# Kernel optimization log

Hardware: AMD Instinct MI355X
Metric: run time of the kernel (lower is better)

Reference implementation:

```python
import jax, jax.numpy as jnp
import numpy as np

B, H, W, DIM = 1, 256, 256, 192
HEADS = 6
K, DIL = 7, 2            # NAttention kernel / dilation
WS, DF = 8, 2            # stripe window size, anchor down factor
AWS = WS // DF           # anchor window size (4)
N1, N2 = WS * WS, AWS * AWS
L = H * W
CPB_HID = 512


def _nbr(size, k, d):
    # 1D neighborhood-attention neighbor indices with dilation (edge-clamped)
    i = np.arange(size); g = i % d; p = i // d
    gsize = size // d  # d divides size
    start = np.clip(p - k // 2, 0, gsize - k)
    nbr_p = start[:, None] + np.arange(k)[None, :]
    nbr = g[:, None] + d * nbr_p                    # absolute key index
    rb = nbr_p - p[:, None] + (k - 1)               # rpb index in [0, 2k-2]
    return nbr.astype(np.int32), rb.astype(np.int32)

NBR_H, RB_H = _nbr(H, K, DIL)
NBR_W, RB_W = _nbr(W, K, DIL)


def _na_attention(q, k, v, rpb):
    # q,k,v: (B, heads, H, W, hd); rpb: (heads, 2K-1, 2K-1)
    bias = rpb[:, RB_H, :]                          # (heads,H,K,2K-1)
    bias = jnp.take(bias, RB_W, axis=3)             # (heads,H,K,W,K)
    bias = jnp.transpose(bias, (0, 1, 3, 2, 4))     # (heads,H,W,K,K)
    logits = []
    for ki in range(K):
        kh = jnp.take(k, NBR_H[:, ki], axis=2)
        for kj in range(K):
            khw = jnp.take(kh, NBR_W[:, kj], axis=3)
            logits.append(jnp.einsum('bnhwc,bnhwc->bnhw', q, khw))
    a = jnp.stack(logits, axis=-1).reshape(*q.shape[:4], K, K) + bias[None]
    a = jax.nn.softmax(a.reshape(*q.shape[:4], K * K), axis=-1).reshape(*q.shape[:4], K, K)
    out = jnp.zeros_like(q)
    for ki in range(K):
        vh = jnp.take(v, NBR_H[:, ki], axis=2)
        for kj in range(K):
            vhw = jnp.take(vh, NBR_W[:, kj], axis=3)
            out = out + a[..., ki, kj, None] * vhw
    return out

na_attention = jax.checkpoint(_na_attention)


def window_partition(x, ws):
    b, h, w, c = x.shape
    x = x.reshape(b, h // ws, ws, w // ws, ws, c)
    return jnp.transpose(x, (0, 1, 3, 2, 4, 5)).reshape(-1, ws * ws, c)


def window_reverse(x, ws, h, w):
    c = x.shape[-1]
    b = x.shape[0] // ((h // ws) * (w // ws))
    x = x.reshape(b, h // ws, w // ws, ws, ws, c)
    return jnp.transpose(x, (0, 1, 3, 2, 4, 5)).reshape(b, h, w, c)


def _l2n(x):
    n = jnp.linalg.norm(x, axis=-1, keepdims=True)
    return x / jnp.maximum(n, 1e-12)


def _affine(attn, table, index, ls, w1, b1, w2):
    # attn: (Bw, heads, Na, Nb)
    attn = attn * jnp.exp(jnp.minimum(ls, float(np.log(100.0))))[None]
    bt = jax.nn.relu(table.reshape(-1, 2) @ w1 + b1) @ w2           # (T, heads)
    bias = bt[index.reshape(-1)].reshape(index.shape[0], index.shape[1], HEADS)
    bias = 16.0 * jax.nn.sigmoid(jnp.transpose(bias, (2, 0, 1)))    # (heads,Na,Nb)
    return attn + bias[None]


def _cos_attn(q, k, v, table, index, ls, w1, b1, w2):
    attn = jnp.einsum('bhnc,bhmc->bhnm', _l2n(q), _l2n(k))
    attn = jax.nn.softmax(_affine(attn, table, index, ls, w1, b1, w2), axis=-1)
    return attn @ v


def _forward(x, h_size, w_size, table, index_a2w, index_w2a, qkv_w, qkv_b,
             anchor_dw_w, anchor_dw_b, anchor_pw_w, anchor_pw_b,
             na_qkv_w, na_qkv_b, na_after_w, na_after_b, na_rpb,
             ls1, cpb1_w1, cpb1_b1, cpb1_w2, ls2, cpb2_w1, cpb2_b1, cpb2_w2,
             proj_w, proj_b):
    Bx, Lx, C = x.shape
    Hs, Ws_ = int(h_size), int(w_size)
    qkv = x @ qkv_w + qkv_b                     # (B,L,3C)
    half = C * 3 // 2
    qkv_window, qkv_stripe = qkv[..., :half], qkv[..., half:]
    # anchor projection: depthwise conv (k=DF+1, stride=DF) + pointwise
    xi = x.reshape(Bx, Hs, Ws_, C)
    a = jax.lax.conv_general_dilated(
        xi, anchor_dw_w, (DF, DF), ((1, 1), (1, 1)),
        dimension_numbers=('NHWC', 'HWIO', 'NHWC'), feature_group_count=C) + anchor_dw_b
    a = a @ anchor_pw_w + anchor_pw_b           # (B, H/DF, W/DF, C//2)
    # ---- neighborhood attention branch ----
    hd = C // HEADS
    xw = qkv_window.reshape(Bx, Hs, Ws_, half)
    q2 = (xw @ na_qkv_w + na_qkv_b).reshape(Bx, Hs, Ws_, 3, HEADS, hd)
    q2 = jnp.transpose(q2, (3, 0, 4, 1, 2, 5))  # (3,B,heads,H,W,hd)
    qn, kn, vn = q2[0] * hd ** -0.5, q2[1], q2[2]
    xna = na_attention(qn, kn, vn, na_rpb)
    xna = jnp.transpose(xna, (0, 2, 3, 1, 4)).reshape(Bx, Hs, Ws_, C)
    xna = (xna @ na_after_w + na_after_b).reshape(Bx, Lx, C // 2)
    # ---- anchor stripe attention branch ----
    qs = window_partition(qkv_stripe.reshape(Bx, Hs, Ws_, half), WS)  # (Bw,N1,1.5C)
    an = window_partition(a, AWS)                                     # (Bw,N2,C//2)
    Bw = qs.shape[0]
    hs = C // 2 // HEADS
    q3 = jnp.transpose(qs.reshape(Bw, N1, 3, HEADS, hs), (2, 0, 3, 1, 4))
    q_s, k_s, v_s = q3[0], q3[1], q3[2]
    an = jnp.transpose(an.reshape(Bw, N2, HEADS, hs), (0, 2, 1, 3))
    x1 = _cos_attn(an, k_s, v_s, table, index_a2w, ls1, cpb1_w1, cpb1_b1, cpb1_w2)
    x2 = _cos_attn(q_s, an, x1, table, index_w2a, ls2, cpb2_w1, cpb2_b1, cpb2_w2)
    x2 = jnp.transpose(x2, (0, 2, 1, 3)).reshape(Bw, N1, C // 2)
    xs = window_reverse(x2, WS, Hs, Ws_).reshape(Bx, Lx, C // 2)
    return jnp.concatenate([xna, xs], axis=-1) @ proj_w + proj_b


def setup_inputs() -> dict:
    key = jax.random.key(0)
    ks = jax.random.split(key, 16)
    f = lambda i, shp, s=0.02: jax.random.normal(ks[i], shp, dtype=jnp.float32) * s
    x = jax.random.normal(ks[0], (B, L, DIM), dtype=jnp.float32)
    # swin-v2 style normalized log-spaced relative coords table
    rc = np.arange(-(WS - 1), WS, dtype=np.float32) / (WS - 1)
    t = np.stack(np.meshgrid(rc, rc, indexing='ij'), axis=-1)[None]
    table = jnp.asarray(np.sign(t) * np.log2(1 + np.abs(t) * 8) / 3.0, dtype=jnp.float32)
    wc = np.arange(WS); ac = np.arange(AWS) * DF
    cw = np.stack(np.meshgrid(wc, wc, indexing='ij'), -1).reshape(-1, 2)
    ca = np.stack(np.meshgrid(ac, ac, indexing='ij'), -1).reshape(-1, 2)
    def _idx(c1, c2):
        d = c1[:, None, :] - c2[None, :, :]
        return jnp.asarray((d[..., 0] + WS - 1) * (2 * WS - 1) + (d[..., 1] + WS - 1), dtype=jnp.int32)
    return {
        'x': x, 'h_size': H, 'w_size': W, 'table': table,
        'index_a2w': _idx(ca, cw), 'index_w2a': _idx(cw, ca),
        'qkv_w': f(1, (DIM, 3 * DIM)), 'qkv_b': jnp.zeros((3 * DIM,), jnp.float32),
        'anchor_dw_w': f(2, (DF + 1, DF + 1, 1, DIM), 0.1),
        'anchor_dw_b': jnp.zeros((DIM,), jnp.float32),
        'anchor_pw_w': f(3, (DIM, DIM // 2)), 'anchor_pw_b': jnp.zeros((DIM // 2,), jnp.float32),
        'na_qkv_w': f(4, (3 * DIM // 2, 3 * DIM)), 'na_qkv_b': jnp.zeros((3 * DIM,), jnp.float32),
        'na_after_w': f(5, (DIM, DIM // 2)), 'na_after_b': jnp.zeros((DIM // 2,), jnp.float32),
        'na_rpb': f(6, (HEADS, 2 * K - 1, 2 * K - 1)),
        'ls1': jnp.log(10.0) * jnp.ones((HEADS, 1, 1), jnp.float32),
        'cpb1_w1': f(7, (2, CPB_HID), 0.1), 'cpb1_b1': jnp.zeros((CPB_HID,), jnp.float32),
        'cpb1_w2': f(8, (CPB_HID, HEADS), 0.1),
        'ls2': jnp.log(10.0) * jnp.ones((HEADS, 1, 1), jnp.float32),
        'cpb2_w1': f(9, (2, CPB_HID), 0.1), 'cpb2_b1': jnp.zeros((CPB_HID,), jnp.float32),
        'cpb2_w2': f(10, (CPB_HID, HEADS), 0.1),
        'proj_w': f(11, (DIM, DIM)), 'proj_b': jnp.zeros((DIM,), jnp.float32),
    }


def reference(x, h_size, w_size, table, index_a2w, index_w2a, qkv_w, qkv_b,
              anchor_dw_w, anchor_dw_b, anchor_pw_w, anchor_pw_b,
              na_qkv_w, na_qkv_b, na_after_w, na_after_b, na_rpb,
              ls1, cpb1_w1, cpb1_b1, cpb1_w2, ls2, cpb2_w1, cpb2_b1, cpb2_w2,
              proj_w, proj_b):
    return _forward(x, h_size, w_size, table, index_a2w, index_w2a, qkv_w, qkv_b,
                    anchor_dw_w, anchor_dw_b, anchor_pw_w, anchor_pw_b,
                    na_qkv_w, na_qkv_b, na_after_w, na_after_b, na_rpb,
                    ls1, cpb1_w1, cpb1_b1, cpb1_w2, ls2, cpb2_w1, cpb2_b1, cpb2_w2,
                    proj_w, proj_b)
```

## Files before the change

kernel.cpp:

```cpp
#include <hip/hip_runtime.h>
#include <math.h>


typedef unsigned short bf16_t;
typedef __attribute__((ext_vector_type(8))) short short8;
typedef __attribute__((ext_vector_type(4))) float f32x4;

__device__ inline float bf2f(bf16_t v) { return __uint_as_float((unsigned)v << 16); }
__device__ inline bf16_t f2bf(float f) {
    unsigned u = __float_as_uint(f);
    unsigned r = (u + 0x7fffu + ((u >> 16) & 1u)) >> 16;
    return (bf16_t)r;
}
__device__ inline float cvt(float v) { return v; }
__device__ inline float cvt(bf16_t v) { return bf2f(v); }
__device__ inline void sto(float* p, float v) { *p = v; }
__device__ inline void sto(bf16_t* p, float v) { *p = f2bf(v); }

__device__ inline void ld_bf8(const bf16_t* p, float* d) {
    uint4 r = *(const uint4*)p;
    d[0] = __uint_as_float(r.x << 16); d[1] = __uint_as_float(r.x & 0xffff0000u);
    d[2] = __uint_as_float(r.y << 16); d[3] = __uint_as_float(r.y & 0xffff0000u);
    d[4] = __uint_as_float(r.z << 16); d[5] = __uint_as_float(r.z & 0xffff0000u);
    d[6] = __uint_as_float(r.w << 16); d[7] = __uint_as_float(r.w & 0xffff0000u);
}
__device__ inline unsigned pk2(float a, float b) {
    return (unsigned)f2bf(a) | ((unsigned)f2bf(b) << 16);
}

template <int KD, int NA, typename TO>
__global__ __launch_bounds__(256) void mfma_gemm_k(
    const bf16_t* __restrict__ A, const bf16_t* __restrict__ Bt,
    const float* __restrict__ bias, TO* __restrict__ C,
    int lda, int ldb, int ldc)
{
    const int t = threadIdx.x;
    const int lane = t & 63, wave = t >> 6;
    const int wr = wave >> 1, wc = wave & 1;
    const int m0 = blockIdx.y * 128 + wr * 64;
    const int n0 = blockIdx.x * 96 + wc * 48;
    const int lm = lane & 15;
    const int q  = lane >> 4;

    f32x4 acc[4][3] = {};
    const bf16_t* ap = A + (size_t)(m0 + lm) * lda + q * 8;
    const bf16_t* bp = Bt + (size_t)(n0 + lm) * ldb + q * 8;

#pragma unroll
    for (int k0 = 0; k0 < KD; k0 += 32) {
        short8 af[4], bf[3];
#pragma unroll
        for (int mi = 0; mi < 4; mi++)
            af[mi] = *(const short8*)(ap + (size_t)(mi * 16) * lda + k0);
#pragma unroll
        for (int ni = 0; ni < 3; ni++)
            bf[ni] = *(const short8*)(bp + (size_t)(ni * 16) * ldb + k0);
#pragma unroll
        for (int mi = 0; mi < 4; mi++)
#pragma unroll
            for (int ni = 0; ni < 3; ni++)
                acc[mi][ni] = __builtin_amdgcn_mfma_f32_16x16x32_bf16(
                    af[mi], bf[ni], acc[mi][ni], 0, 0, 0);
    }

#pragma unroll
    for (int mi = 0; mi < 4; mi++) {
#pragma unroll
        for (int ni = 0; ni < 3; ni++) {
            int col = n0 + ni * 16 + lm;
            float bv = bias[col];
            if (NA) {
                int which = col / 192;
                int hh = (col % 192) / 32;
                int d  = col % 32;
                size_t pbase = ((size_t)which * 6 + hh) * ((size_t)65536 * 32) + d;
#pragma unroll
                for (int r = 0; r < 4; r++) {
                    int row = m0 + mi * 16 + q * 4 + r;
                    int ii = row >> 8, jj = row & 255;
                    int par = ((ii & 1) << 1) | (jj & 1);
                    int pix = par * 16384 + (ii >> 1) * 128 + (jj >> 1);
                    sto(&C[pbase + (size_t)pix * 32], acc[mi][ni][r] + bv);
                }
            } else {
#pragma unroll
                for (int r = 0; r < 4; r++) {
                    int row = m0 + mi * 16 + q * 4 + r;
                    sto(&C[(size_t)row * ldc + col], acc[mi][ni][r] + bv);
                }
            }
        }
    }
}

__global__ __launch_bounds__(256) void cvt_bf16_k(
    const float* __restrict__ src, bf16_t* __restrict__ dst, int n8)
{
    int tid = blockIdx.x * 256 + threadIdx.x;
    if (tid >= n8) return;
    float4 a = ((const float4*)src)[tid * 2];
    float4 b = ((const float4*)src)[tid * 2 + 1];
    uint4 o;
    o.x = pk2(a.x, a.y); o.y = pk2(a.z, a.w);
    o.z = pk2(b.x, b.y); o.w = pk2(b.z, b.w);
    ((uint4*)dst)[tid] = o;
}

__global__ __launch_bounds__(256) void tcvt_k(
    const float* __restrict__ W, bf16_t* __restrict__ Wt,
    int Kd, int N, int ld, int coloff)
{
    int tid = blockIdx.x * 256 + threadIdx.x;
    if (tid >= Kd * N) return;
    int k = tid % Kd, n = tid / Kd;
    Wt[tid] = f2bf(W[(size_t)k * ld + coloff + n]);
}

__global__ __launch_bounds__(256) void tpose_qkvw_k(
    const float* __restrict__ W, float* __restrict__ WT)
{
    int tid = blockIdx.x * 256 + threadIdx.x;
    if (tid >= 288 * 192) return;
    int k = tid % 192, j = tid / 192;
    WT[tid] = W[(size_t)k * 576 + j];
}

__global__ __launch_bounds__(256) void fold_wna_t_k(
    const float* __restrict__ qkv_wT, const float* __restrict__ na_qkv_w,
    bf16_t* __restrict__ Wna_t)
{
    int tid = blockIdx.x * 256 + threadIdx.x;
    if (tid >= 576 * 192) return;
    int k = tid % 192, n = tid / 192;
    float acc = 0.f;
    for (int j = 0; j < 288; j++)
        acc += qkv_wT[j * 192 + k] * na_qkv_w[j * 576 + n];
    Wna_t[tid] = f2bf(acc);
}

__global__ __launch_bounds__(256) void fold_bna_k(
    const float* __restrict__ qkv_b, const float* __restrict__ na_qkv_w,
    const float* __restrict__ na_qkv_b, float* __restrict__ bna)
{
    int j = blockIdx.x * 256 + threadIdx.x;
    if (j >= 576) return;
    float acc = na_qkv_b[j];
    for (int k = 0; k < 288; k++)
        acc += qkv_b[k] * na_qkv_w[k * 576 + j];
    bna[j] = acc;
}

__global__ __launch_bounds__(256) void cpb_k(
    const float* __restrict__ table, const float* __restrict__ w1,
    const float* __restrict__ b1, const float* __restrict__ w2,
    float* __restrict__ bt)
{
    int tid = blockIdx.x * 256 + threadIdx.x;
    if (tid >= 225 * 6) return;
    int h = tid % 6, t = tid / 6;
    float t0 = table[t * 2], t1 = table[t * 2 + 1];
    float acc = 0.f;
    for (int m = 0; m < 512; m++) {
        float hv = t0 * w1[m] + t1 * w1[512 + m] + b1[m];
        hv = fmaxf(hv, 0.f);
        acc += hv * w2[m * 6 + h];
    }
    bt[tid] = acc;
}

__global__ __launch_bounds__(256) void sigb_k(
    const float* __restrict__ bt, const int* __restrict__ idx,
    float* __restrict__ bp)
{
    int tid = blockIdx.x * 256 + threadIdx.x;
    if (tid >= 6144) return;
    int h = tid >> 10, p = tid & 1023;
    bp[tid] = 16.0f / (1.0f + __expf(-bt[idx[p] * 6 + h]));
}

__global__ __launch_bounds__(256) void sigb1T_k(
    const float* __restrict__ bt, const int* __restrict__ idx,
    float* __restrict__ bp)
{
    int tid = blockIdx.x * 256 + threadIdx.x;
    if (tid >= 6144) return;
    int h = tid >> 10, p = tid & 1023;
    int m = p >> 4, n2 = p & 15;
    bp[tid] = 16.0f / (1.0f + __expf(-bt[idx[n2 * 64 + m] * 6 + h]));
}

#define BM 64
#define BN 64
#define BKK 16
template <typename TA, typename TO>
__global__ __launch_bounds__(256) void gemm_k(
    const TA* __restrict__ A, const float* __restrict__ B,
    const float* __restrict__ bias, TO* __restrict__ C,
    int M, int N, int Kd, int lda, int ldb, int ldc)
{
    __shared__ float As[BKK][BM + 1];
    __shared__ float Bs[BKK][BN + 1];
    const int t  = threadIdx.x;
    const int tx = t & 15, ty = t >> 4;
    const int m0 = blockIdx.y * BM, n0 = blockIdx.x * BN;
    float acc[4][4] = {};

    for (int k0 = 0; k0 < Kd; k0 += BKK) {
#pragma unroll
        for (int i = 0; i < 4; i++) {
            int m = (t >> 4) + i * 16;
            int k = t & 15;
            int gm = m0 + m, gk = k0 + k;
            As[k][m] = (gm < M && gk < Kd) ? cvt(A[(size_t)gm * lda + gk]) : 0.f;
        }
#pragma unroll
        for (int i = 0; i < 4; i++) {
            int k = (t >> 6) + i * 4;
            int n = t & 63;
            int gk = k0 + k, gn = n0 + n;
            Bs[k][n] = (gk < Kd && gn < N) ? B[(size_t)gk * ldb + gn] : 0.f;
        }
        __syncthreads();
#pragma unroll
        for (int k = 0; k < BKK; k++) {
            float a[4], b[4];
#pragma unroll
            for (int i = 0; i < 4; i++) a[i] = As[k][ty * 4 + i];
#pragma unroll
            for (int j = 0; j < 4; j++) b[j] = Bs[k][tx * 4 + j];
#pragma unroll
            for (int i = 0; i < 4; i++)
#pragma unroll
                for (int j = 0; j < 4; j++) acc[i][j] += a[i] * b[j];
        }
        __syncthreads();
    }
#pragma unroll
    for (int i = 0; i < 4; i++) {
        int gm = m0 + ty * 4 + i;
        if (gm >= M) continue;
#pragma unroll
        for (int j = 0; j < 4; j++) {
            int gn = n0 + tx * 4 + j;
            if (gn >= N) continue;
            sto(&C[(size_t)gm * ldc + gn], acc[i][j] + bias[gn]);
        }
    }
}

__global__ __launch_bounds__(256) void dwconv_k(
    const float* __restrict__ x, const float* __restrict__ w,
    const float* __restrict__ b, float* __restrict__ adw)
{
    int tid = blockIdx.x * 256 + threadIdx.x;
    if (tid >= 16384 * 48) return;
    int c4 = tid % 48;
    int p = tid / 48;
    int ow = p & 127, oh = p >> 7;
    int c = c4 * 4;
    float4 s = *(const float4*)(b + c);
#pragma unroll
    for (int kh = 0; kh < 3; kh++) {
        int ih = oh * 2 - 1 + kh;
        if (ih < 0 || ih >= 256) continue;
#pragma unroll
        for (int kw = 0; kw < 3; kw++) {
            int iw = ow * 2 - 1 + kw;
            if (iw < 0 || iw >= 256) continue;
            float4 xv = *(const float4*)(x + (size_t)(ih * 256 + iw) * 192 + c);
            float4 wv = *(const float4*)(w + (kh * 3 + kw) * 192 + c);
            s.x += xv.x * wv.x; s.y += xv.y * wv.y;
            s.z += xv.z * wv.z; s.w += xv.w * wv.w;
        }
    }
    *(float4*)(adw + (size_t)p * 192 + c) = s;
}

__global__ __launch_bounds__(256) void na_attn_k(
    const bf16_t* __restrict__ nap, const float* __restrict__ rpb,
    bf16_t* __restrict__ outp)
{
    __shared__ float rpb_s[176];
    __shared__ __align__(16) unsigned P_s[4][16][20];

    const int t = threadIdx.x;
    const int wv = t >> 6, lane = t & 63;
    const int lm = lane & 15, lq = lane >> 4;
    const int z = blockIdx.z;
    const int h = z >> 2, par = z & 3;

    if (t < 169) rpb_s[t] = rpb[h * 169 + t];
    __syncthreads();

    const int pi  = blockIdx.y;
    const int pj0 = blockIdx.x * 64 + wv * 16;
    const int si  = min(max(pi - 3, 0), 121);
    const int rbh0 = si - pi + 6;
    const int c0  = min(max(pj0 - 3, 0), 121) & ~7;

    const size_t plane = (size_t)65536 * 32;
    const size_t poff  = (size_t)(par * 16384) * 32;
    const bf16_t* qpl = nap + (size_t)h * plane + poff;
    const bf16_t* kpl = nap + (size_t)(6 + h) * plane + poff;
    const bf16_t* vpl = nap + (size_t)(12 + h) * plane + poff;

    const short8 qf = *(const short8*)(qpl + ((size_t)(pi * 128 + pj0 + lm)) * 32 + lq * 8);

    int offc[4][2]; bool vm[4][2];
#pragma unroll
    for (int r = 0; r < 4; r++) {
        int q = lq * 4 + r, pj = pj0 + q;
        int sj = min(max(pj - 3, 0), 121);
#pragma unroll
        for (int t2 = 0; t2 < 2; t2++) {
            int c = c0 + 2 * lm + t2;
            vm[r][t2] = (c >= sj) && (c <= sj + 6);
            offc[r][t2] = min(max(c - pj + 6, 0), 12);
        }
    }
    const int kc0 = min(c0 + 2 * lm,     127) * 64;
    const int kc1 = min(c0 + 2 * lm + 1, 127) * 64;
    int vcoff[8];
#pragma unroll
    for (int i = 0; i < 8; i++) vcoff[i] = min(c0 + lq * 8 + i, 127) * 64;

    const float scale = 0.17677669529663687f;
    f32x4 o0 = {}, o1 = {};
    float sums[4] = {0.f, 0.f, 0.f, 0.f};
    const f32x4 zz = {};

#pragma unroll 2
    for (int rr = 0; rr < 7; rr++) {
        const size_t rb2 = (size_t)((si + rr) * 128) * 64;
        const char* krow = (const char*)kpl + rb2;
        const char* vrow = (const char*)vpl + rb2;

        short8 kf0 = *(const short8*)(krow + kc0 + lq * 16);
        short8 kf1 = *(const short8*)(krow + kc1 + lq * 16);
        f32x4 s0 = __builtin_amdgcn_mfma_f32_16x16x32_bf16(qf, kf0, zz, 0, 0, 0);
        f32x4 s1 = __builtin_amdgcn_mfma_f32_16x16x32_bf16(qf, kf1, zz, 0, 0, 0);

        const float* br = rpb_s + (rbh0 + rr) * 13;
        float e0[4], e1[4];
#pragma unroll
        for (int r = 0; r < 4; r++) {
            float a0 = __expf(fmaf(s0[r], scale, br[offc[r][0]]));
            float a1 = __expf(fmaf(s1[r], scale, br[offc[r][1]]));
            a0 = vm[r][0] ? a0 : 0.f;
            a1 = vm[r][1] ? a1 : 0.f;
            e0[r] = a0; e1[r] = a1;
            sums[r] += a0 + a1;
        }
#pragma unroll
        for (int r = 0; r < 4; r++) {
            unsigned pr;
            asm("v_cvt_pk_bf16_f32 %0, %1, %2" : "=v"(pr) : "v"(e0[r]), "v"(e1[r]));
            P_s[wv][lq * 4 + r][lm] = pr;
        }
        const short8 pf = *(const short8*)((const bf16_t*)P_s[wv][lm] + lq * 8);

        short8 vf0, vf1;
        const char* v0b = vrow + lm * 2;
        const char* v1b = vrow + 32 + lm * 2;
#pragma unroll
        for (int i = 0; i < 8; i++) {
            ((bf16_t*)&vf0)[i] = *(const bf16_t*)(v0b + vcoff[i]);
            ((bf16_t*)&vf1)[i] = *(const bf16_t*)(v1b + vcoff[i]);
        }
        o0 = __builtin_amdgcn_mfma_f32_16x16x32_bf16(pf, vf0, o0, 0, 0, 0);
        o1 = __builtin_amdgcn_mfma_f32_16x16x32_bf16(pf, vf1, o1, 0, 0, 0);
    }

#pragma unroll
    for (int r = 0; r < 4; r++) {
        float s = sums[r];
        s += __shfl_xor(s, 1, 64);
        s += __shfl_xor(s, 2, 64);
        s += __shfl_xor(s, 4, 64);
        s += __shfl_xor(s, 8, 64);
        sums[r] = 1.0f / s;
    }

    const int gi = par >> 1, gj = par & 1;
    const int i0 = pi * 2 + gi;
    bf16_t* ob = outp + ((size_t)i0 * 256 + gj) * 192 + h * 32 + lm;
#pragma unroll
    for (int r = 0; r < 4; r++) {
        int q = lq * 4 + r;
        size_t px = (size_t)(pj0 + q) * 2 * 192;
        ob[px]      = f2bf(o0[r] * sums[r]);
        ob[px + 16] = f2bf(o1[r] * sums[r]);
    }
}

__global__ __launch_bounds__(256) void attn1_k(
    const float* __restrict__ apw,
    const bf16_t* __restrict__ qkvs,
    const float* __restrict__ b1pT,
    const float* __restrict__ ls1,
    float* __restrict__ x1)
{
    __shared__ float bT_s[1024];
    __shared__ __align__(16) unsigned P_s[4][16][36];

    const int t = threadIdx.x;
    const int wv = t >> 6, lane = t & 63;
    const int lm = lane & 15, lq = lane >> 4;
    const int h = blockIdx.y;
    const int w = blockIdx.x * 4 + wv;
    const int wi = w >> 5, wj = w & 31;

#pragma unroll
    for (int i = 0; i < 4; i++) bT_s[i * 256 + t] = b1pT[h * 1024 + i * 256 + t];
    __syncthreads();

    const float scale = __expf(fminf(ls1[h], 4.605170185988091f));

    short8 af = {};
    float an2 = 0.f;
    {
        int ay = wi * 4 + (lm >> 2), ax = wj * 4 + (lm & 3);
        const float* ap = apw + (size_t)(ay * 128 + ax) * 96 + h * 16;
        if (lq < 2) {
            float4 v0 = *(const float4*)(ap + lq * 8);
            float4 v1 = *(const float4*)(ap + lq * 8 + 4);
            float vs[8] = {v0.x, v0.y, v0.z, v0.w, v1.x, v1.y, v1.z, v1.w};
            unsigned* au = (unsigned*)&af;
#pragma unroll
            for (int j2 = 0; j2 < 4; j2++) {
                unsigned u = pk2(vs[2 * j2], vs[2 * j2 + 1]);
                au[j2] = u;
                float lo = __uint_as_float(u << 16);
                float hi = __uint_as_float(u & 0xffff0000u);
                an2 += lo * lo + hi * hi;
            }
        }
    }
    an2 += __shfl_xor(an2, 16, 64);
    an2 += __shfl_xor(an2, 32, 64);
    const float sa = scale / fmaxf(sqrtf(an2), 1e-12f);

    const f32x4 zz = {};
    f32x4 o = {};
    float sum = 0.f;

#pragma unroll
    for (int g = 0; g < 2; g++) {
#pragma unroll
        for (int tt = 0; tt < 2; tt++) {
            const int tile = g * 2 + tt;
            int py = wi * 8 + tile * 2 + (lm >> 3);
            int px = wj * 8 + (lm & 7);
            const bf16_t* kp = qkvs + (size_t)(py * 256 + px) * 288 + 96 + h * 16;
            short8 kf = {};
            float kn2 = 0.f;
            float klo[4], khi[4];
            if (lq < 2) {
                uint4 kr = *(const uint4*)(kp + lq * 8);
                unsigned ku[4] = {kr.x, kr.y, kr.z, kr.w};
#pragma unroll
                for (int j2 = 0; j2 < 4; j2++) {
                    klo[j2] = __uint_as_float(ku[j2] << 16);
                    khi[j2] = __uint_as_float(ku[j2] & 0xffff0000u);
                    kn2 += klo[j2] * klo[j2] + khi[j2] * khi[j2];
                }
            }
            kn2 += __shfl_xor(kn2, 16, 64);
            kn2 += __shfl_xor(kn2, 32, 64);
            float rk = 1.0f / fmaxf(sqrtf(kn2), 1e-12f);
            if (lq < 2) {
                unsigned* kuo = (unsigned*)&kf;
#pragma unroll
                for (int j2 = 0; j2 < 4; j2++)
                    kuo[j2] = pk2(klo[j2] * rk, khi[j2] * rk);
            }
            f32x4 s = __builtin_amdgcn_mfma_f32_16x16x32_bf16(kf, af, zz, 0, 0, 0);
            float e[4];
#pragma unroll
            for (int r = 0; r < 4; r++) {
                e[r] = __expf(fmaf(s[r], sa,
                              bT_s[((tile * 16 + lq * 4 + r) << 4) + lm]));
                sum += e[r];
            }
            P_s[wv][lm][tile * 8 + lq * 2]     = pk2(e[0], e[1]);
            P_s[wv][lm][tile * 8 + lq * 2 + 1] = pk2(e[2], e[3]);
        }
        const short8 pf = *(const short8*)&P_s[wv][lm][g * 16 + lq * 4];
        short8 vf;
        int pyv = wi * 8 + g * 4 + lq;
        const bf16_t* vrow = qkvs + (size_t)(pyv * 256 + wj * 8) * 288 + 192 + h * 16 + lm;
#pragma unroll
        for (int i = 0; i < 8; i++)
            ((bf16_t*)&vf)[i] = vrow[(size_t)i * 288];
        o = __builtin_amdgcn_mfma_f32_16x16x32_bf16(pf, vf, o, 0, 0, 0);
    }

    sum += __shfl_xor(sum, 16, 64);
    sum += __shfl_xor(sum, 32, 64);
    const float inv = 1.0f / sum;
    float* xp = x1 + ((size_t)w * 6 + h) * 256;
#pragma unroll
    for (int r = 0; r < 4; r++) {
        float iv = __shfl(inv, lq * 4 + r, 64);
        xp[(lq * 4 + r) * 16 + lm] = o[r] * iv;
    }
}

__global__ __launch_bounds__(256) void attn2_k(
    const float* __restrict__ apw,
    const bf16_t* __restrict__ qkvs,
    const float* __restrict__ b2p,
    const float* __restrict__ ls2,
    const float* __restrict__ x1,
    bf16_t* __restrict__ cat)
{
    int tid = blockIdx.x * 256 + threadIdx.x;
    if (tid >= 1024 * 6 * 64) return;
    int n1 = tid & 63;
    int h = (tid >> 6) % 6;
    int w = tid / 384;
    int wi = w >> 5, wj = w & 31;
    float scale = __expf(fminf(ls2[h], 4.605170185988091f));

    int qy = wi * 8 + (n1 >> 3), qx = wj * 8 + (n1 & 7);
    const bf16_t* qp = qkvs + (size_t)(qy * 256 + qx) * 288 + h * 16;
    float qv[16];
    ld_bf8(qp, qv); ld_bf8(qp + 8, qv + 8);
    float nrm = 0.f;
#pragma unroll
    for (int d = 0; d < 16; d++) nrm += qv[d] * qv[d];
    float innorm = 1.0f / fmaxf(sqrtf(nrm), 1e-12f);
#pragma unroll
    for (int d = 0; d < 16; d++) qv[d] *= innorm;

    const float* bp = b2p + h * 1024 + n1 * 16;
    float sum = 0.f;
    float acc[16] = {};
#pragma unroll
    for (int m = 0; m < 16; m++) {
        int ay = wi * 4 + (m >> 2), ax = wj * 4 + (m & 3);
        const float* ap = apw + (size_t)(ay * 128 + ax) * 96 + h * 16;
        float dot = 0.f, kn = 0.f;
#pragma unroll
        for (int d = 0; d < 16; d += 4) {
            float4 v = *(const float4*)(ap + d);
            dot += qv[d] * v.x + qv[d + 1] * v.y + qv[d + 2] * v.z + qv[d + 3] * v.w;
            kn += v.x * v.x + v.y * v.y + v.z * v.z + v.w * v.w;
        }
        dot *= 1.0f / fmaxf(sqrtf(kn), 1e-12f);
        float e = __expf(fmaf(dot, scale, bp[m]));
        sum += e;
        const float* vp = x1 + ((size_t)w * 6 + h) * 256 + m * 16;
#pragma unroll
        for (int d = 0; d < 16; d += 4) {
            float4 v = *(const float4*)(vp + d);
            acc[d] += e * v.x; acc[d + 1] += e * v.y;
            acc[d + 2] += e * v.z; acc[d + 3] += e * v.w;
        }
    }
    float inv = 1.0f / sum;
#pragma unroll
    for (int d = 0; d < 16; d++) acc[d] *= inv;
    bf16_t* op = cat + (size_t)(qy * 256 + qx) * 192 + 96 + h * 16;
    uint4 o0, o1;
    o0.x = pk2(acc[0], acc[1]);   o0.y = pk2(acc[2], acc[3]);
    o0.z = pk2(acc[4], acc[5]);   o0.w = pk2(acc[6], acc[7]);
    o1.x = pk2(acc[8], acc[9]);   o1.y = pk2(acc[10], acc[11]);
    o1.z = pk2(acc[12], acc[13]); o1.w = pk2(acc[14], acc[15]);
    *(uint4*)(op) = o0;
    *(uint4*)(op + 8) = o1;
}

extern "C" void kernel_launch(void* const* d_in, const int* in_sizes, int n_in,
                              void* d_out, int out_size, void* d_ws, size_t ws_size,
                              hipStream_t stream) {
    const float* x          = (const float*)d_in[0];
    const float* table      = (const float*)d_in[3];
    const int*   idx_a2w    = (const int*)d_in[4];
    const int*   idx_w2a    = (const int*)d_in[5];
    const float* qkv_w      = (const float*)d_in[6];
    const float* qkv_b      = (const float*)d_in[7];
    const float* adw_w      = (const float*)d_in[8];
    const float* adw_b      = (const float*)d_in[9];
    const float* apw_w      = (const float*)d_in[10];
    const float* apw_b      = (const float*)d_in[11];
    const float* na_qkv_w   = (const float*)d_in[12];
    const float* na_qkv_b   = (const float*)d_in[13];
    const float* na_after_w = (const float*)d_in[14];
    const float* na_after_b = (const float*)d_in[15];
    const float* na_rpb     = (const float*)d_in[16];
    const float* ls1        = (const float*)d_in[17];
    const float* cpb1_w1    = (const float*)d_in[18];
    const float* cpb1_b1    = (const float*)d_in[19];
    const float* cpb1_w2    = (const float*)d_in[20];
    const float* ls2        = (const float*)d_in[21];
    const float* cpb2_w1    = (const float*)d_in[22];
    const float* cpb2_b1    = (const float*)d_in[23];
    const float* cpb2_w2    = (const float*)d_in[24];
    const float* proj_w     = (const float*)d_in[25];
    const float* proj_b     = (const float*)d_in[26];
    float* out = (float*)d_out;
    (void)in_sizes; (void)n_in; (void)out_size; (void)ws_size;

    char* base = (char*)d_ws;
    size_t off = 0;
    auto alloc = [&](size_t bytes) {
        off = (off + 255) & ~(size_t)255;
        void* p = base + off; off += bytes; return p;
    };
    float*  bna    = (float*)alloc(576 * 4);
    float*  bt1    = (float*)alloc(225 * 6 * 4);
    float*  bt2    = (float*)alloc(225 * 6 * 4);
    float*  b1pT   = (float*)alloc(6144 * 4);
    float*  b2p    = (float*)alloc(6144 * 4);
    float*  qkv_wT = (float*)alloc(288 * 192 * 4);
    bf16_t* Wna_t  = (bf16_t*)alloc(576 * 192 * 2);
    bf16_t* Ws_t   = (bf16_t*)alloc(288 * 192 * 2);
    bf16_t* Waft_t = (bf16_t*)alloc(96 * 192 * 2);
    bf16_t* Wproj_t= (bf16_t*)alloc(192 * 192 * 2);
    bf16_t* qkvs   = (bf16_t*)alloc((size_t)65536 * 288 * 2);
    char*   naR    = (char*)alloc((size_t)65536 * 576 * 2);
    char*   R      = (char*)alloc((size_t)65536 * 192 * 2);
    float*  apw    = (float*)alloc((size_t)16384 * 96 * 4);
    bf16_t* naqkv   = (bf16_t*)naR;
    float*  x1      = (float*)naR;
    bf16_t* cat     = (bf16_t*)(naR + (8 << 20));
    bf16_t* xb      = (bf16_t*)R;
    float*  adw     = (float*)R;
    bf16_t* xna_pre = (bf16_t*)R;

    tpose_qkvw_k<<<216, 256, 0, stream>>>(qkv_w, qkv_wT);
    fold_wna_t_k<<<432, 256, 0, stream>>>(qkv_wT, na_qkv_w, Wna_t);
    fold_bna_k<<<3, 256, 0, stream>>>(qkv_b, na_qkv_w, na_qkv_b, bna);
    cpb_k<<<6, 256, 0, stream>>>(table, cpb1_w1, cpb1_b1, cpb1_w2, bt1);
    cpb_k<<<6, 256, 0, stream>>>(table, cpb2_w1, cpb2_b1, cpb2_w2, bt2);
    sigb1T_k<<<24, 256, 0, stream>>>(bt1, idx_a2w, b1pT);
    sigb_k<<<24, 256, 0, stream>>>(bt2, idx_w2a, b2p);
    tcvt_k<<<216, 256, 0, stream>>>(qkv_w, Ws_t, 192, 288, 576, 288);
    tcvt_k<<<72, 256, 0, stream>>>(na_after_w, Waft_t, 192, 96, 96, 0);
    tcvt_k<<<144, 256, 0, stream>>>(proj_w, Wproj_t, 192, 192, 192, 0);
    cvt_bf16_k<<<6144, 256, 0, stream>>>(x, xb, 65536 * 192 / 8);

    mfma_gemm_k<192, 0, bf16_t><<<dim3(3, 512), 256, 0, stream>>>(
        xb, Ws_t, qkv_b + 288, qkvs, 192, 192, 288);

    mfma_gemm_k<192, 1, bf16_t><<<dim3(6, 512), 256, 0, stream>>>(
        xb, Wna_t, bna, naqkv, 192, 192, 576);

    dwconv_k<<<3072, 256, 0, stream>>>(x, adw_w, adw_b, adw);
    gemm_k<float, float><<<dim3(2, 256), 256, 0, stream>>>(
        adw, apw_w, apw_b, apw, 16384, 96, 192, 192, 96, 96);

    na_attn_k<<<dim3(2, 128, 24), 256, 0, stream>>>(naqkv, na_rpb, xna_pre);

    mfma_gemm_k<192, 0, bf16_t><<<dim3(1, 512), 256, 0, stream>>>(
        xna_pre, Waft_t, na_after_b, cat, 192, 192, 192);

    attn1_k<<<dim3(256, 6), 256, 0, stream>>>(apw, qkvs, b1pT, ls1, x1);
    attn2_k<<<1536, 256, 0, stream>>>(apw, qkvs, b2p, ls2, x1, cat);

    mfma_gemm_k<192, 0, float><<<dim3(2, 512), 256, 0, stream>>>(
        cat, Wproj_t, proj_b, out, 192, 192, 192);
}
```

Before: 600.8 us.

## Store NA value planes transposed and swizzle attention blocks across XCDs

The NA QKV GEMM epilogue now writes the V planes in a channel-major (transposed) layout per head and parity. The neighborhood-attention kernel can then fetch each V fragment with one 16-byte vector load instead of eight scalar bf16 gathers. The attention launch is also flattened to a 1D grid, with block ids remapped so consecutive work lands on the same XCD for better L2 locality. In exchange, the GEMM's V stores become strided, with a 16384-element stride per channel, which may weaken write coalescing. Out-of-window V reads are clamped only at the plane end and rely on zero softmax weights.

```diff
diff --git a/kernel.cpp b/kernel.cpp
--- a/kernel.cpp
+++ b/kernel.cpp
@@ -73,14 +73,20 @@
                 int which = col / 192;
                 int hh = (col % 192) / 32;
                 int d  = col % 32;
-                size_t pbase = ((size_t)which * 6 + hh) * ((size_t)65536 * 32) + d;
 #pragma unroll
                 for (int r = 0; r < 4; r++) {
                     int row = m0 + mi * 16 + q * 4 + r;
                     int ii = row >> 8, jj = row & 255;
                     int par = ((ii & 1) << 1) | (jj & 1);
-                    int pix = par * 16384 + (ii >> 1) * 128 + (jj >> 1);
-                    sto(&C[pbase + (size_t)pix * 32], acc[mi][ni][r] + bv);
+                    int pixin = (ii >> 1) * 128 + (jj >> 1);
+                    size_t addr;
+                    if (which == 2)
+                        addr = (((size_t)(12 + hh) * 4 + par) << 19)
+                             + ((size_t)d << 14) + pixin;
+                    else
+                        addr = ((size_t)which * 6 + hh) * 2097152 + d
+                             + ((size_t)(par * 16384 + pixin) << 5);
+                    sto(&C[addr], acc[mi][ni][r] + bv);
                 }
             } else {
 #pragma unroll
@@ -283,17 +289,22 @@
     __shared__ float rpb_s[176];
     __shared__ __align__(16) unsigned P_s[4][16][20];
 
+    const int bid  = blockIdx.x;
+    const int work = (bid & 7) * 768 + (bid >> 3);
+    const int z    = work >> 8;
+    const int rem  = work & 255;
+    const int pi   = rem >> 1;
+    const int xh   = rem & 1;
+
     const int t = threadIdx.x;
     const int wv = t >> 6, lane = t & 63;
     const int lm = lane & 15, lq = lane >> 4;
-    const int z = blockIdx.z;
     const int h = z >> 2, par = z & 3;
 
     if (t < 169) rpb_s[t] = rpb[h * 169 + t];
     __syncthreads();
 
-    const int pi  = blockIdx.y;
-    const int pj0 = blockIdx.x * 64 + wv * 16;
+    const int pj0 = xh * 64 + wv * 16;
     const int si  = min(max(pi - 3, 0), 121);
     const int rbh0 = si - pi + 6;
     const int c0  = min(max(pj0 - 3, 0), 121) & ~7;
@@ -302,7 +313,7 @@
     const size_t poff  = (size_t)(par * 16384) * 32;
     const bf16_t* qpl = nap + (size_t)h * plane + poff;
     const bf16_t* kpl = nap + (size_t)(6 + h) * plane + poff;
-    const bf16_t* vpl = nap + (size_t)(12 + h) * plane + poff;
+    const bf16_t* vtpl = nap + (((size_t)(12 + h) * 4 + par) << 19);
 
     const short8 qf = *(const short8*)(qpl + ((size_t)(pi * 128 + pj0 + lm)) * 32 + lq * 8);
 
@@ -320,9 +331,9 @@
     }
     const int kc0 = min(c0 + 2 * lm,     127) * 64;
     const int kc1 = min(c0 + 2 * lm + 1, 127) * 64;
-    int vcoff[8];
-#pragma unroll
-    for (int i = 0; i < 8; i++) vcoff[i] = min(c0 + lq * 8 + i, 127) * 64;
+    const int vcol = c0 + (lq << 3);
+    const size_t vb0 = (size_t)lm * 16384;
+    const size_t vb1 = (size_t)(lm + 16) * 16384;
 
     const float scale = 0.17677669529663687f;
     f32x4 o0 = {}, o1 = {};
@@ -331,9 +342,7 @@
 
 #pragma unroll 2
     for (int rr = 0; rr < 7; rr++) {
-        const size_t rb2 = (size_t)((si + rr) * 128) * 64;
-        const char* krow = (const char*)kpl + rb2;
-        const char* vrow = (const char*)vpl + rb2;
+        const char* krow = (const char*)kpl + (size_t)((si + rr) * 128) * 64;
 
         short8 kf0 = *(const short8*)(krow + kc0 + lq * 16);
         short8 kf1 = *(const short8*)(krow + kc1 + lq * 16);
@@ -359,14 +368,10 @@
         }
         const short8 pf = *(const short8*)((const bf16_t*)P_s[wv][lm] + lq * 8);
 
-        short8 vf0, vf1;
-        const char* v0b = vrow + lm * 2;
-        const char* v1b = vrow + 32 + lm * 2;
-#pragma unroll
-        for (int i = 0; i < 8; i++) {
-            ((bf16_t*)&vf0)[i] = *(const bf16_t*)(v0b + vcoff[i]);
-            ((bf16_t*)&vf1)[i] = *(const bf16_t*)(v1b + vcoff[i]);
-        }
+        int rowo = min((si + rr) * 128 + vcol, 16376);
+        short8 vf0 = *(const short8*)(vtpl + vb0 + rowo);
+        short8 vf1 = *(const short8*)(vtpl + vb1 + rowo);
+
         o0 = __builtin_amdgcn_mfma_f32_16x16x32_bf16(pf, vf0, o0, 0, 0, 0);
         o1 = __builtin_amdgcn_mfma_f32_16x16x32_bf16(pf, vf1, o1, 0, 0, 0);
     }
@@ -651,7 +656,7 @@
     gemm_k<float, float><<<dim3(2, 256), 256, 0, stream>>>(
         adw, apw_w, apw_b, apw, 16384, 96, 192, 192, 96, 96);
 
-    na_attn_k<<<dim3(2, 128, 24), 256, 0, stream>>>(naqkv, na_rpb, xna_pre);
+    na_attn_k<<<6144, 256, 0, stream>>>(naqkv, na_rpb, xna_pre);
 
     mfma_gemm_k<192, 0, bf16_t><<<dim3(1, 512), 256, 0, stream>>>(
         xna_pre, Waft_t, na_after_b, cat, 192, 192, 192);
```

After: 638.8 us. 1.06x slower.
